# Optimization experiments

Measured on AMD Instinct MI355X. Metric: run time of the kernel, lower is better.

## Reference

```python
import jax, jax.numpy as jnp
import numpy as np

M, K, N = 64, 4096, 11008
GROUPSIZE = 64
MAXQ = 7  # 3-bit
ZERO = (MAXQ + 1) // 2  # symmetric zero point = 4


def setup_inputs() -> dict:
    key = jax.random.key(0)
    k1, k2, k3 = jax.random.split(key, 3)
    A = jax.random.normal(k1, (M, K), dtype=jnp.float32)
    # 3-bit quantized weight codes in [0, 7], logical shape (k, n)
    q = jax.random.randint(k2, (K, N), 0, MAXQ + 1, dtype=jnp.int32)
    # per-group scales, shape (k // groupsize, n); keep positive like real scales
    s = jax.random.uniform(k3, (K // GROUPSIZE, N), dtype=jnp.float32, minval=0.005, maxval=0.02)
    return {"A": A, "q": q, "s": s}


def reference(A, q, s):
    k, n = q.shape
    g = k // s.shape[0]  # groupsize (64)
    # dequantize: W[i, j] = (q[i, j] - 4) * s[i // g, j]
    centered = (q - ZERO).astype(s.dtype)              # (k, n)
    W = (centered.reshape(-1, g, n) * s[:, None, :]).reshape(k, n)
    # C = A @ W  (fused dequant-GEMM in the CUDA kernel)
    return jnp.matmul(A, W)
```

## Files before the change

kernel.cpp:

```cpp
#include <hip/hip_runtime.h>

#define K_ 4096
#define N_ 11008
#define M_ 64
#define SB 4
#define CB 86
#define BK 32
#define BN 128
#define KBAND (K_ / SB)
#define NSTEP (KBAND / BK)
#define NBUF 4

typedef __attribute__((ext_vector_type(8))) short bf16x8;
typedef __attribute__((ext_vector_type(4))) float f32x4;
typedef __attribute__((ext_vector_type(4))) unsigned uint4v;
typedef __attribute__((ext_vector_type(4))) float float4v;
typedef __attribute__((ext_vector_type(4))) unsigned short ushort4v;

static __device__ __forceinline__ unsigned rne_bits(float f) {
  unsigned u = __builtin_bit_cast(unsigned, f);
  return u + 0x7fffu + ((u >> 16) & 1u);
}
static __device__ __forceinline__ unsigned pack_bf16(float lo, float hi) {
  return (rne_bits(hi) & 0xffff0000u) | (rne_bits(lo) >> 16);
}
static __device__ __forceinline__ unsigned short bf16_1(float f) {
  return (unsigned short)(rne_bits(f) >> 16);
}
static __device__ __forceinline__ float bf16_to_f32(unsigned short u) {
  return __builtin_bit_cast(float, (unsigned)u << 16);
}

__global__ __launch_bounds__(256) void cvtA_frag_kernel(
    const float* __restrict__ A, unsigned* __restrict__ Apf) {
  const int kt = blockIdx.x;
  const int mt = threadIdx.x >> 6;
  const int l  = threadIdx.x & 63;
  const int row = mt * 16 + (l & 15);
  const int kk  = kt * 32 + (l >> 4) * 8;
  const float* ap = A + (size_t)row * K_ + kk;
  uint4v b = { pack_bf16(ap[0], ap[1]), pack_bf16(ap[2], ap[3]),
               pack_bf16(ap[4], ap[5]), pack_bf16(ap[6], ap[7]) };
  *reinterpret_cast<uint4v*>(Apf + ((size_t)(kt * 4 + mt) * 64 + l) * 4) = b;
}

__global__ __launch_bounds__(512, 4) void dq_gemm_pipe(
    const int* __restrict__ q, const float* __restrict__ s,
    const unsigned* __restrict__ Apf, unsigned short* __restrict__ P) {
  __shared__ int qtile[NBUF][BK * BN];
  __shared__ int atile[NBUF][1024];

  const int tid = threadIdx.x;
  const int l   = tid & 63;
  const int w   = tid >> 6;
  const int fr  = l & 15;
  const int lg  = l >> 4;
  const int cb  = blockIdx.x % CB;
  const int sb  = blockIdx.x / CB;
  const int n0  = cb * BN;
  const int k0  = sb * KBAND;
  const int cw  = w * 16;

  float scv[NSTEP / 2];
  #pragma unroll
  for (int g = 0; g < NSTEP / 2; ++g)
    scv[g] = s[(size_t)((k0 >> 6) + g) * N_ + n0 + cw + fr];

  f32x4 acc[4] = {f32x4{0,0,0,0}, f32x4{0,0,0,0}, f32x4{0,0,0,0}, f32x4{0,0,0,0}};

  auto stage = [&](int buf, int kst) {
    #pragma unroll
    for (int i = 0; i < 2; ++i) {
      const int rbase = w * 4 + i * 2;
      const int row   = rbase + (l >> 5);
      const int rot   = ((row >> 3) & 3) * 8;
      const int c4    = (4 * l) & 127;
      const int src   = (c4 - rot) & 127;
      const int* gp   = q + (size_t)(kst + row) * N_ + n0 + src;
      __builtin_amdgcn_global_load_lds(
          (const __attribute__((address_space(1))) unsigned*)gp,
          (__attribute__((address_space(3))) unsigned*)&qtile[buf][rbase * BN],
          16, 0, 0);
    }
    const unsigned* ab = Apf + (size_t)(kst >> 5) * 1024 + w * 128;
    #pragma unroll
    for (int i = 0; i < 2; ++i) {
      __builtin_amdgcn_global_load_lds(
          (const __attribute__((address_space(1))) unsigned*)(ab + i * 64 + l),
          (__attribute__((address_space(3))) unsigned*)&atile[buf][w * 128 + i * 64],
          4, 0, 0);
    }
  };

  auto compute = [&](int buf, float sc) {
    bf16x8 af[4];
    #pragma unroll
    for (int mt = 0; mt < 4; ++mt)
      af[mt] = *reinterpret_cast<const bf16x8*>(&atile[buf][mt * 256 + l * 4]);
    const float sn = -4.0f * sc;
    const int rot = 8 * lg;
    const int ci  = (cw + fr + rot) & 127;
    unsigned pk[4];
    #pragma unroll
    for (int p = 0; p < 4; ++p) {
      const int r0 = 8 * lg + 2 * p;
      const int c0 = qtile[buf][r0 * BN + ci];
      const int c1 = qtile[buf][(r0 + 1) * BN + ci];
      pk[p] = pack_bf16(fmaf((float)c0, sc, sn), fmaf((float)c1, sc, sn));
    }
    uint4v bv = {pk[0], pk[1], pk[2], pk[3]};
    const bf16x8 bfrag = __builtin_bit_cast(bf16x8, bv);
    #pragma unroll
    for (int mt = 0; mt < 4; ++mt)
      acc[mt] = __builtin_amdgcn_mfma_f32_16x16x32_bf16(af[mt], bfrag, acc[mt],
                                                        0, 0, 0);
  };

  stage(0, k0);
  stage(1, k0 + BK);
  stage(2, k0 + 2 * BK);

  #pragma unroll
  for (int st = 0; st < NSTEP - 2; ++st) {
    asm volatile("s_waitcnt vmcnt(8)" ::: "memory");
    __builtin_amdgcn_s_barrier();
    __builtin_amdgcn_sched_barrier(0);
    if (st + 3 < NSTEP) stage((st + 3) & 3, k0 + (st + 3) * BK);
    compute(st & 3, scv[st >> 1]);
  }
  asm volatile("s_waitcnt vmcnt(4)" ::: "memory");
  __builtin_amdgcn_s_barrier();
  __builtin_amdgcn_sched_barrier(0);
  compute((NSTEP - 2) & 3, scv[(NSTEP - 2) >> 1]);

  asm volatile("s_waitcnt vmcnt(0)" ::: "memory");
  __builtin_amdgcn_s_barrier();
  __builtin_amdgcn_sched_barrier(0);
  compute((NSTEP - 1) & 3, scv[(NSTEP - 1) >> 1]);

  unsigned short* Pb = P + (size_t)(cb * SB + sb) * M_ * BN;
  #pragma unroll
  for (int mt = 0; mt < 4; ++mt)
    #pragma unroll
    for (int j = 0; j < 4; ++j)
      Pb[(mt * 16 + 4 * lg + j) * BN + cw + fr] = bf16_1(acc[mt][j]);
}

__global__ __launch_bounds__(256) void reduce_kernel(
    const unsigned short* __restrict__ P, float* __restrict__ out) {
  const int flat = blockIdx.x * 256 + threadIdx.x;
  const int cb = flat >> 11;
  const int r  = flat & 2047;
  const int m  = r >> 5;
  const int cq = (r & 31) * 4;
  const unsigned short* p = P + ((size_t)cb * SB * M_ + m) * BN + cq;
  float s0 = 0.f, s1 = 0.f, s2 = 0.f, s3 = 0.f;
  #pragma unroll
  for (int sb = 0; sb < SB; ++sb) {
    ushort4v v = *reinterpret_cast<const ushort4v*>(p + (size_t)sb * M_ * BN);
    s0 += bf16_to_f32(v[0]);
    s1 += bf16_to_f32(v[1]);
    s2 += bf16_to_f32(v[2]);
    s3 += bf16_to_f32(v[3]);
  }
  float4v o = {s0, s1, s2, s3};
  *reinterpret_cast<float4v*>(out + (size_t)m * N_ + cb * BN + cq) = o;
}

__global__ __launch_bounds__(512, 8) void dq_gemm_basic(
    const int* __restrict__ q, const float* __restrict__ s,
    const float* __restrict__ Af, float* __restrict__ out) {
  __shared__ int tile[2][BK * BN];

  const int tid = threadIdx.x;
  const int l   = tid & 63;
  const int w   = tid >> 6;
  const int fr  = l & 15;
  const int lg  = l >> 4;
  const int cb  = blockIdx.x % CB;
  const int sb  = blockIdx.x / CB;
  const int n0  = cb * BN;
  const int k0  = sb * KBAND;
  const int cw  = w * 16;

  f32x4 acc[4] = {f32x4{0,0,0,0}, f32x4{0,0,0,0}, f32x4{0,0,0,0}, f32x4{0,0,0,0}};

  auto stage = [&](int buf, int kst) {
    #pragma unroll
    for (int i = 0; i < 2; ++i) {
      const int rbase = w * 4 + i * 2;
      const int row   = rbase + (l >> 5);
      const int rot   = ((row >> 3) & 3) * 8;
      const int c4    = (4 * l) & 127;
      const int src   = (c4 - rot) & 127;
      const int* gp   = q + (size_t)(kst + row) * N_ + n0 + src;
      __builtin_amdgcn_global_load_lds(
          (const __attribute__((address_space(1))) unsigned*)gp,
          (__attribute__((address_space(3))) unsigned*)&tile[buf][rbase * BN],
          16, 0, 0);
    }
  };

  auto compute = [&](int buf, int kst) {
    const float sc = s[(size_t)(kst >> 6) * N_ + n0 + cw + fr];
    bf16x8 af[4];
    #pragma unroll
    for (int mt = 0; mt < 4; ++mt) {
      const float* ap = Af + (size_t)(mt * 16 + fr) * K_ + kst + 8 * lg;
      float4v v0 = *reinterpret_cast<const float4v*>(ap);
      float4v v1 = *reinterpret_cast<const float4v*>(ap + 4);
      uint4v b = { pack_bf16(v0[0], v0[1]), pack_bf16(v0[2], v0[3]),
                   pack_bf16(v1[0], v1[1]), pack_bf16(v1[2], v1[3]) };
      af[mt] = __builtin_bit_cast(bf16x8, b);
    }
    const float sn = -4.0f * sc;
    const int rot = 8 * lg;
    const int ci  = (cw + fr + rot) & 127;
    unsigned pk[4];
    #pragma unroll
    for (int p = 0; p < 4; ++p) {
      const int r0 = 8 * lg + 2 * p;
      const int c0 = tile[buf][r0 * BN + ci];
      const int c1 = tile[buf][(r0 + 1) * BN + ci];
      pk[p] = pack_bf16(fmaf((float)c0, sc, sn), fmaf((float)c1, sc, sn));
    }
    uint4v bv = {pk[0], pk[1], pk[2], pk[3]};
    const bf16x8 bfrag = __builtin_bit_cast(bf16x8, bv);
    #pragma unroll
    for (int mt = 0; mt < 4; ++mt)
      acc[mt] = __builtin_amdgcn_mfma_f32_16x16x32_bf16(af[mt], bfrag, acc[mt],
                                                        0, 0, 0);
  };

  stage(0, k0);
  __syncthreads();
  for (int st = 0; st < NSTEP; ++st) {
    const int kst = k0 + st * BK;
    if (st + 1 < NSTEP) stage((st + 1) & 1, kst + BK);
    compute(st & 1, kst);
    __syncthreads();
  }

  #pragma unroll
  for (int mt = 0; mt < 4; ++mt)
    #pragma unroll
    for (int j = 0; j < 4; ++j)
      atomicAdd(out + (size_t)(mt * 16 + 4 * lg + j) * N_ + n0 + cw + fr,
                acc[mt][j]);
}

extern "C" void kernel_launch(void* const* d_in, const int* in_sizes, int n_in,
                              void* d_out, int out_size, void* d_ws, size_t ws_size,
                              hipStream_t stream) {
  const float* A = (const float*)d_in[0];
  const int*   q = (const int*)d_in[1];
  const float* s = (const float*)d_in[2];
  float* out = (float*)d_out;

  const size_t apBytes = (size_t)128 * 1024 * sizeof(unsigned);
  const size_t pBytes  = (size_t)CB * SB * M_ * BN * sizeof(unsigned short);
  const size_t needFull = apBytes + pBytes;

  if (ws_size >= needFull) {
    unsigned* Apf = (unsigned*)d_ws;
    unsigned short* P = (unsigned short*)((char*)d_ws + apBytes);
    hipLaunchKernelGGL(cvtA_frag_kernel, dim3(128), dim3(256), 0, stream,
                       A, Apf);
    hipLaunchKernelGGL(dq_gemm_pipe, dim3(CB * SB), dim3(512), 0, stream,
                       q, s, Apf, P);
    hipLaunchKernelGGL(reduce_kernel, dim3(688), dim3(256), 0, stream, P, out);
  } else {
    hipMemsetAsync(d_out, 0, (size_t)M_ * N_ * sizeof(float), stream);
    hipLaunchKernelGGL(dq_gemm_basic, dim3(CB * SB), dim3(512), 0, stream,
                       q, s, A, out);
  }
}
```

Baseline: 46.15 us.

## Fuse A bf16 conversion into GEMM, double K-split, reorder compute before staging

Removes the separate cvtA_frag_kernel launch: the GEMM now streams fp32 A tiles directly into LDS with a rotated slot swizzle and converts them to bf16 fragments in registers. The K-split factor goes from 4 to 8, doubling the block count, with occupancy bounds lowered to 2 per CU because LDS per block grows. In the main loop, compute now runs before the next prefetch is issued, and the wait counts are adjusted to match. The cost removed is a kernel launch plus the Apf round trip; in exchange every block re-converts A, A traffic doubles in bytes, and more partials must be reduced.

```diff
diff --git a/kernel.cpp b/kernel.cpp
--- a/kernel.cpp
+++ b/kernel.cpp
@@ -3,7 +3,7 @@
 #define K_ 4096
 #define N_ 11008
 #define M_ 64
-#define SB 4
+#define SB 8
 #define CB 86
 #define BK 32
 #define BN 128
@@ -31,24 +31,11 @@
   return __builtin_bit_cast(float, (unsigned)u << 16);
 }
 
-__global__ __launch_bounds__(256) void cvtA_frag_kernel(
-    const float* __restrict__ A, unsigned* __restrict__ Apf) {
-  const int kt = blockIdx.x;
-  const int mt = threadIdx.x >> 6;
-  const int l  = threadIdx.x & 63;
-  const int row = mt * 16 + (l & 15);
-  const int kk  = kt * 32 + (l >> 4) * 8;
-  const float* ap = A + (size_t)row * K_ + kk;
-  uint4v b = { pack_bf16(ap[0], ap[1]), pack_bf16(ap[2], ap[3]),
-               pack_bf16(ap[4], ap[5]), pack_bf16(ap[6], ap[7]) };
-  *reinterpret_cast<uint4v*>(Apf + ((size_t)(kt * 4 + mt) * 64 + l) * 4) = b;
-}
-
-__global__ __launch_bounds__(512, 4) void dq_gemm_pipe(
+__global__ __launch_bounds__(512, 2) void dq_gemm_pipe(
     const int* __restrict__ q, const float* __restrict__ s,
-    const unsigned* __restrict__ Apf, unsigned short* __restrict__ P) {
-  __shared__ int qtile[NBUF][BK * BN];
-  __shared__ int atile[NBUF][1024];
+    const float* __restrict__ A, unsigned short* __restrict__ P) {
+  __shared__ int   qtile[NBUF][BK * BN];
+  __shared__ float atile[NBUF][64 * 32];
 
   const int tid = threadIdx.x;
   const int l   = tid & 63;
@@ -82,21 +69,30 @@
           (__attribute__((address_space(3))) unsigned*)&qtile[buf][rbase * BN],
           16, 0, 0);
     }
-    const unsigned* ab = Apf + (size_t)(kst >> 5) * 1024 + w * 128;
-    #pragma unroll
-    for (int i = 0; i < 2; ++i) {
+    {
+      const int arow   = w * 8 + (l >> 3);
+      const int slot_g = ((l & 7) - (l >> 3)) & 7;
+      const float* ap  = A + (size_t)arow * K_ + kst + slot_g * 4;
       __builtin_amdgcn_global_load_lds(
-          (const __attribute__((address_space(1))) unsigned*)(ab + i * 64 + l),
-          (__attribute__((address_space(3))) unsigned*)&atile[buf][w * 128 + i * 64],
-          4, 0, 0);
+          (const __attribute__((address_space(1))) unsigned*)ap,
+          (__attribute__((address_space(3))) unsigned*)&atile[buf][w * 256],
+          16, 0, 0);
     }
   };
 
   auto compute = [&](int buf, float sc) {
     bf16x8 af[4];
     #pragma unroll
-    for (int mt = 0; mt < 4; ++mt)
-      af[mt] = *reinterpret_cast<const bf16x8*>(&atile[buf][mt * 256 + l * 4]);
+    for (int mt = 0; mt < 4; ++mt) {
+      const int arow = mt * 16 + fr;
+      const int s0   = (lg * 2 + (fr & 7)) & 7;
+      const int s1   = (lg * 2 + 1 + (fr & 7)) & 7;
+      float4v va = *reinterpret_cast<const float4v*>(&atile[buf][arow * 32 + s0 * 4]);
+      float4v vb = *reinterpret_cast<const float4v*>(&atile[buf][arow * 32 + s1 * 4]);
+      uint4v b = { pack_bf16(va[0], va[1]), pack_bf16(va[2], va[3]),
+                   pack_bf16(vb[0], vb[1]), pack_bf16(vb[2], vb[3]) };
+      af[mt] = __builtin_bit_cast(bf16x8, b);
+    }
     const float sn = -4.0f * sc;
     const int rot = 8 * lg;
     const int ci  = (cw + fr + rot) & 127;
@@ -122,13 +118,13 @@
 
   #pragma unroll
   for (int st = 0; st < NSTEP - 2; ++st) {
-    asm volatile("s_waitcnt vmcnt(8)" ::: "memory");
+    asm volatile("s_waitcnt vmcnt(6)" ::: "memory");
     __builtin_amdgcn_s_barrier();
     __builtin_amdgcn_sched_barrier(0);
+    compute(st & 3, scv[st >> 1]);
     if (st + 3 < NSTEP) stage((st + 3) & 3, k0 + (st + 3) * BK);
-    compute(st & 3, scv[st >> 1]);
-  }
-  asm volatile("s_waitcnt vmcnt(4)" ::: "memory");
+  }
+  asm volatile("s_waitcnt vmcnt(3)" ::: "memory");
   __builtin_amdgcn_s_barrier();
   __builtin_amdgcn_sched_barrier(0);
   compute((NSTEP - 2) & 3, scv[(NSTEP - 2) >> 1]);
@@ -257,17 +253,12 @@
   const float* s = (const float*)d_in[2];
   float* out = (float*)d_out;
 
-  const size_t apBytes = (size_t)128 * 1024 * sizeof(unsigned);
-  const size_t pBytes  = (size_t)CB * SB * M_ * BN * sizeof(unsigned short);
-  const size_t needFull = apBytes + pBytes;
-
-  if (ws_size >= needFull) {
-    unsigned* Apf = (unsigned*)d_ws;
-    unsigned short* P = (unsigned short*)((char*)d_ws + apBytes);
-    hipLaunchKernelGGL(cvtA_frag_kernel, dim3(128), dim3(256), 0, stream,
-                       A, Apf);
+  const size_t pBytes = (size_t)CB * SB * M_ * BN * sizeof(unsigned short);
+
+  if (ws_size >= pBytes) {
+    unsigned short* P = (unsigned short*)d_ws;
     hipLaunchKernelGGL(dq_gemm_pipe, dim3(CB * SB), dim3(512), 0, stream,
-                       q, s, Apf, P);
+                       q, s, A, P);
     hipLaunchKernelGGL(reduce_kernel, dim3(688), dim3(256), 0, stream, P, out);
   } else {
     hipMemsetAsync(d_out, 0, (size_t)M_ * N_ * sizeof(float), stream);
```

After: 55.06 us. 19.3% more time.
